# Optimization experiments

Measured on AMD Instinct MI355X. Metric: run time of the kernel, lower is better.

## Reference

```python
import jax, jax.numpy as jnp
import numpy as np

B, L, D, H = 4, 8192, 1024, 8
Dh = D // H
EPS = 1e-4
PAD = 1  # circular padding on each side, kernel_size=3, stride=1


def setup_inputs() -> dict:
    key = jax.random.key(0)
    k1, k2, k3, k4, k5 = jax.random.split(key, 5)
    return {
        "x": jax.random.normal(k1, (B, L, D), dtype=jnp.float32),
        "hash_w": jax.random.normal(k2, (H, Dh, 2), dtype=jnp.float32) * 0.05,
        "hash_b": jax.random.normal(k3, (H, 2), dtype=jnp.float32) * 0.05,
        "conv_w": jax.random.normal(k4, (D, D // H, 3), dtype=jnp.float32) * 0.05,
        "conv_b": jax.random.normal(k5, (D,), dtype=jnp.float32) * 0.05,
    }


def reference(x, hash_w, hash_b, conv_w, conv_b):
    # x: [B, L, D]
    xh = x.reshape(B, L, H, Dh)
    # per-head 2-dim hash projection, concatenated as [x0,y0,x1,y1,...] on last dim
    proj = jnp.einsum('blhd,hdk->blhk', xh, hash_w) + hash_b  # [B,L,H,2]
    proj = proj.reshape(B, L, 2 * H)
    # faithful to torch.split(projected, n_heads, dim=2): first H vs last H channels
    h_x, h_y = proj[..., :H], proj[..., H:]
    angles = jnp.arctan(h_x / (h_y + EPS))  # [B,L,H]
    idx = jnp.argsort(angles, axis=1)       # [B,L,H] permutation along L per (b,h)
    # gather: reorder tokens per head
    xs = jnp.take_along_axis(xh, idx[..., None], axis=1)  # [B,L,H,Dh]
    # grouped circular Conv1d over the sorted sequence
    xc = xs.reshape(B, L, D).swapaxes(1, 2)               # [B,D,L]
    xc = jnp.pad(xc, ((0, 0), (0, 0), (PAD, PAD)), mode='wrap')
    y = jax.lax.conv_general_dilated(
        xc, conv_w, window_strides=(1,), padding='VALID',
        dimension_numbers=('NCH', 'OIH', 'NCH'), feature_group_count=H)
    y = y + conv_b[None, :, None]                          # [B,D,L]
    y = y.swapaxes(1, 2).reshape(B, L, H, Dh)
    # scatter back to original token order == gather with inverse permutation
    inv = jnp.argsort(idx, axis=1)
    out = jnp.take_along_axis(y, inv[..., None], axis=1)
    return out.reshape(B, L, D)
```

## Files before the change

### kernel.cpp

```cpp
#include <hip/hip_runtime.h>
#include <math.h>

#define LL 8192
#define DD 1024
#define DH 128

typedef unsigned long long u64;
typedef __attribute__((ext_vector_type(8))) short bf16x8;
typedef __attribute__((ext_vector_type(4))) float f32x4;

__device__ __forceinline__ unsigned f2bf(float f) {
  unsigned u = __float_as_uint(f);
  u = (u + 0x7fffu + ((u >> 16) & 1u)) >> 16;
  return u;
}

__device__ __forceinline__ float fdlibm_atanf(float x) {
#pragma clang fp contract(off)
  const float atanhi0 = __uint_as_float(0x3eed6338u);
  const float atanhi1 = __uint_as_float(0x3f490fdau);
  const float atanhi2 = __uint_as_float(0x3f7b985eu);
  const float atanhi3 = __uint_as_float(0x3fc90fdau);
  const float atanlo0 = __uint_as_float(0x31ac3769u);
  const float atanlo1 = __uint_as_float(0x33222168u);
  const float atanlo2 = __uint_as_float(0x33140fb4u);
  const float atanlo3 = __uint_as_float(0x33a22168u);
  const float aT0 = __uint_as_float(0x3eaaaaa9u);
  const float aT1 = __uint_as_float(0xbe4cca98u);
  const float aT2 = __uint_as_float(0x3e11f50du);
  const float aT3 = __uint_as_float(0xbdda1247u);
  const float aT4 = __uint_as_float(0x3d7cac25u);
  unsigned hx = __float_as_uint(x);
  unsigned ix = hx & 0x7fffffffu;
  int id;
  if (ix >= 0x4c800000u) {
    if (ix > 0x7f800000u) return x + x;
    float z = atanhi3 + atanlo3;
    return (hx >> 31) ? -z : z;
  }
  if (ix < 0x3ee00000u) {
    if (ix < 0x39800000u) return x;
    id = -1;
  } else {
    x = fabsf(x);
    if (ix < 0x3f980000u) {
      if (ix < 0x3f300000u) { id = 0; x = (2.0f * x - 1.0f) / (2.0f + x); }
      else                  { id = 1; x = (x - 1.0f) / (x + 1.0f); }
    } else {
      if (ix < 0x401c0000u) { id = 2; x = (x - 1.5f) / (1.0f + 1.5f * x); }
      else                  { id = 3; x = -1.0f / x; }
    }
  }
  float z = x * x;
  float w = z * z;
  float s1 = z * (aT0 + w * (aT2 + w * aT4));
  float s2 = w * (aT1 + w * aT3);
  if (id < 0) return x - x * (s1 + s2);
  float r;
  if (id == 0)      r = atanhi0 - ((x * (s1 + s2) - atanlo0) - x);
  else if (id == 1) r = atanhi1 - ((x * (s1 + s2) - atanlo1) - x);
  else if (id == 2) r = atanhi2 - ((x * (s1 + s2) - atanlo2) - x);
  else              r = atanhi3 - ((x * (s1 + s2) - atanlo3) - x);
  return (hx >> 31) ? -r : r;
}

__global__ __launch_bounds__(256) void k_keys(const float* __restrict__ x,
                                              const float* __restrict__ hw,
                                              const float* __restrict__ hb,
                                              u64* __restrict__ ks,
                                              const float* __restrict__ cw,
                                              unsigned short* __restrict__ wb) {
  __shared__ float2 wL[128][8];
  __shared__ float projL[32][16];
  const int tid = threadIdx.x;
  const float2* hw2 = (const float2*)hw;
  for (int i = tid; i < 1024; i += 256) {
    int hh = i >> 7, dd = i & 127;
    wL[dd][hh] = hw2[i];
  }
  __syncthreads();
  const int r = tid >> 3;
  const int h = tid & 7;
  const int m = blockIdx.x * 32 + r;
  const int b = m >> 13, l = m & (LL - 1);
  const float4* xp = (const float4*)(x + (size_t)m * DD + h * DH);
  float a0 = 0.f, a1 = 0.f;
#pragma unroll
  for (int q = 0; q < 32; ++q) {
    float4 v = xp[q];
    float2 w0 = wL[q * 4 + 0][h];
    float2 w1 = wL[q * 4 + 1][h];
    float2 w2 = wL[q * 4 + 2][h];
    float2 w3 = wL[q * 4 + 3][h];
    a0 = fmaf(v.x, w0.x, a0); a1 = fmaf(v.x, w0.y, a1);
    a0 = fmaf(v.y, w1.x, a0); a1 = fmaf(v.y, w1.y, a1);
    a0 = fmaf(v.z, w2.x, a0); a1 = fmaf(v.z, w2.y, a1);
    a0 = fmaf(v.w, w3.x, a0); a1 = fmaf(v.w, w3.y, a1);
  }
  projL[r][h * 2 + 0] = a0;
  projL[r][h * 2 + 1] = a1;
  __syncthreads();
  const int j = h;
  float px = projL[r][j] + hb[j];
  float py = projL[r][8 + j] + hb[8 + j];
  float den = py + 1e-4f;
  float ratio = px / den;
  float angle = fdlibm_atanf(ratio);
  unsigned am = __float_as_uint(angle);
  am = (am & 0x80000000u) ? ~am : (am | 0x80000000u);
  ks[((size_t)b * 8 + j) * LL + l] = ((u64)am << 13) | (u64)l;
  {
    int base = blockIdx.x * 384;
    for (int g = base + tid; g < base + 384; g += 256) {
      int hh = g / 49152;
      int rem = g % 49152;
      int kk = rem >> 12;
      int rem2 = rem & 4095;
      int n = rem2 >> 9;
      int rem3 = rem2 & 511;
      int l2 = rem3 >> 3;
      int j2 = rem3 & 7;
      int k = kk * 32 + ((l2 >> 4) * 8) + j2;
      int o = n * 16 + (l2 & 15);
      int t = k >> 7, i2 = k & 127;
      wb[g] = (unsigned short)f2bf(cw[((size_t)(hh * 128 + o)) * 384 + i2 * 3 + t]);
    }
  }
}

__global__ __launch_bounds__(256) void k_sort_loc512(u64* __restrict__ ks) {
  __shared__ u64 sk[512];
  const int blk = blockIdx.x;
  const int seg = blk >> 4, c = blk & 15;
  u64* base = ks + (size_t)seg * LL + c * 512;
  const int tid = threadIdx.x;
  sk[tid] = base[tid];
  sk[tid + 256] = base[tid + 256];
  __syncthreads();
  const int cb = c * 512;
  for (int size = 2; size <= 512; size <<= 1) {
    for (int stride = size >> 1; stride > 0; stride >>= 1) {
      int i = 2 * tid - (tid & (stride - 1));
      int j = i + stride;
      bool up = (((cb + i) & size) == 0);
      u64 a = sk[i], d = sk[j];
      if ((a > d) == up) { sk[i] = d; sk[j] = a; }
      __syncthreads();
    }
  }
  base[tid] = sk[tid];
  base[tid + 256] = sk[tid + 256];
}

__global__ __launch_bounds__(1024) void k_sort_loc2k(u64* __restrict__ ks) {
  __shared__ u64 sk[2048];
  const int blk = blockIdx.x;
  const int seg = blk >> 2, c = blk & 3;
  u64* base = ks + (size_t)seg * LL + c * 2048;
  const int tid = threadIdx.x;
  sk[tid] = base[tid];
  sk[tid + 1024] = base[tid + 1024];
  __syncthreads();
  const int cb = c * 2048;
  for (int size = 1024; size <= 2048; size <<= 1) {
    for (int stride = size >> 1; stride > 0; stride >>= 1) {
      int i = 2 * tid - (tid & (stride - 1));
      int j = i + stride;
      bool up = (((cb + i) & size) == 0);
      u64 a = sk[i], d = sk[j];
      if ((a > d) == up) { sk[i] = d; sk[j] = a; }
      __syncthreads();
    }
  }
  base[tid] = sk[tid];
  base[tid + 1024] = sk[tid + 1024];
}

__global__ __launch_bounds__(1024) void k_sort_t4k(u64* __restrict__ ks) {
  __shared__ u64 sk[4096];
  const int blk = blockIdx.x;
  const int seg = blk >> 1, c = blk & 1;
  u64* base = ks + (size_t)seg * LL + c * 4096;
  const int tid = threadIdx.x;
#pragma unroll
  for (int i = 0; i < 4; ++i) sk[tid + i * 1024] = base[tid + i * 1024];
  __syncthreads();
  const int cb = c * 4096;
  for (int stride = 2048; stride > 0; stride >>= 1) {
#pragma unroll
    for (int pp = 0; pp < 2; ++pp) {
      int p = tid + pp * 1024;
      int i = 2 * p - (p & (stride - 1));
      int j = i + stride;
      bool up = (((cb + i) & 4096) == 0);
      u64 a = sk[i], d = sk[j];
      if ((a > d) == up) { sk[i] = d; sk[j] = a; }
    }
    __syncthreads();
  }
#pragma unroll
  for (int i = 0; i < 4; ++i) base[tid + i * 1024] = sk[tid + i * 1024];
}

__global__ __launch_bounds__(1024) void k_sort_tailg8(const u64* __restrict__ ks,
                                                      int* __restrict__ perm) {
  __shared__ u64 sk[2048];
  const int blk = blockIdx.x;
  const int seg = blk >> 2, c = blk & 3;
  const u64* base = ks + (size_t)seg * LL;
  const int tid = threadIdx.x;
#pragma unroll
  for (int s = 0; s < 2; ++s) {
    int i = tid + s * 1024;
    u64 e0 = base[i], e1 = base[i + 2048], e2 = base[i + 4096], e3 = base[i + 6144];
    u64 tt;
    if (e0 > e2) { tt = e0; e0 = e2; e2 = tt; }
    if (e1 > e3) { tt = e1; e1 = e3; e3 = tt; }
    if (e0 > e1) { tt = e0; e0 = e1; e1 = tt; }
    if (e2 > e3) { tt = e2; e2 = e3; e3 = tt; }
    sk[i] = (c == 0) ? e0 : (c == 1) ? e1 : (c == 2) ? e2 : e3;
  }
  __syncthreads();
  for (int stride = 1024; stride > 0; stride >>= 1) {
    int i = 2 * tid - (tid & (stride - 1));
    int j = i + stride;
    u64 a = sk[i], d = sk[j];
    if (a > d) { sk[i] = d; sk[j] = a; }
    __syncthreads();
  }
  int* dst = perm + (size_t)seg * LL + c * 2048;
  dst[tid] = (int)(sk[tid] & (u64)(LL - 1));
  dst[tid + 1024] = (int)(sk[tid + 1024] & (u64)(LL - 1));
}

__global__ __launch_bounds__(256) void k_conv(const float* __restrict__ x,
                                              const unsigned short* __restrict__ wb,
                                              const float* __restrict__ bias,
                                              const int* __restrict__ perm,
                                              float* __restrict__ out) {
  __shared__ short Xs[66 * 136];
  __shared__ short Ws[8 * 64 * 8];
  __shared__ int Ps2[66];
  const int tid = threadIdx.x;
  const int bid = blockIdx.x;
  const int tile = bid & 127;
  const int h = (bid >> 7) & 7;
  const int b = bid >> 10;
  const int r0 = tile * 64;
  const int* pbh = perm + ((size_t)b * 8 + h) * LL;
  if (tid < 66) Ps2[tid] = pbh[(r0 + tid - 1 + LL) & (LL - 1)];
  const uint4* wsrc = (const uint4*)(wb + (size_t)h * 49152);
  uint4 wr0 = wsrc[tid];
  uint4 wr1 = wsrc[tid + 256];
  __syncthreads();
  {
    const int ln = tid & 31;
    for (int j = (tid >> 5); j < 66; j += 8) {
      int src = Ps2[j];
      float4 v = ((const float4*)(x + ((size_t)(b * LL + src)) * DD + h * DH))[ln];
      uint2 pk;
      pk.x = f2bf(v.x) | (f2bf(v.y) << 16);
      pk.y = f2bf(v.z) | (f2bf(v.w) << 16);
      *(uint2*)(Xs + j * 136 + ln * 4) = pk;
    }
  }
  const int w = tid >> 6;
  const int l = tid & 63;
  const int arow = w * 16 + (l & 15);
  const int acol = (l >> 4) * 8;
  f32x4 acc[8];
#pragma unroll
  for (int n = 0; n < 8; ++n) acc[n] = (f32x4){0.f, 0.f, 0.f, 0.f};
  uint4* Ws16 = (uint4*)Ws;
  for (int kk = 0; kk < 12; ++kk) {
    __syncthreads();
    Ws16[tid] = wr0;
    Ws16[tid + 256] = wr1;
    __syncthreads();
    if (kk < 11) {
      wr0 = wsrc[(kk + 1) * 512 + tid];
      wr1 = wsrc[(kk + 1) * 512 + tid + 256];
    }
    bf16x8 af = *(const bf16x8*)(Xs + (arow + (kk >> 2)) * 136 + (kk & 3) * 32 + acol);
#pragma unroll
    for (int n = 0; n < 8; ++n) {
      bf16x8 bf_ = *(const bf16x8*)(Ws + (n * 64 + l) * 8);
      acc[n] = __builtin_amdgcn_mfma_f32_16x16x32_bf16(af, bf_, acc[n], 0, 0, 0);
    }
  }
  int dsts[4];
#pragma unroll
  for (int reg = 0; reg < 4; ++reg) dsts[reg] = Ps2[1 + w * 16 + (l >> 4) * 4 + reg];
#pragma unroll
  for (int n = 0; n < 8; ++n) {
    int o = h * DH + n * 16 + (l & 15);
    float bv = bias[o];
#pragma unroll
    for (int reg = 0; reg < 4; ++reg) {
      out[((size_t)(b * LL + dsts[reg])) * DD + o] = acc[n][reg] + bv;
    }
  }
}

extern "C" void kernel_launch(void* const* d_in, const int* in_sizes, int n_in,
                              void* d_out, int out_size, void* d_ws, size_t ws_size,
                              hipStream_t stream) {
  const float* x  = (const float*)d_in[0];
  const float* hw = (const float*)d_in[1];
  const float* hb = (const float*)d_in[2];
  const float* cw = (const float*)d_in[3];
  const float* cb = (const float*)d_in[4];
  float* out = (float*)d_out;
  u64* ks   = (u64*)d_ws;
  int* perm = (int*)((char*)d_ws + (2u << 20));
  unsigned short* wbp = (unsigned short*)((char*)d_ws + (3u << 20));

  k_keys<<<1024, 256, 0, stream>>>(x, hw, hb, ks, cw, wbp);
  k_sort_loc512<<<512, 256, 0, stream>>>(ks);
  k_sort_loc2k<<<128, 1024, 0, stream>>>(ks);
  k_sort_t4k<<<64, 1024, 0, stream>>>(ks);
  k_sort_tailg8<<<128, 1024, 0, stream>>>(ks, perm);
  k_conv<<<4096, 256, 0, stream>>>(x, wbp, cb, perm, out);
}
```

Baseline: 118.3 us.

## Cache bf16 per-head copy of x in keys kernel for conv gather

The keys kernel, which already reads all of x, now also converts it to bf16 and writes a head-major [B,H,L,Dh] copy into workspace, staged through a swizzled shared-memory tile for coalesced stores. The conv kernel then gathers permuted rows from this half-size contiguous copy instead of re-reading fp32 x and converting. This halves the bytes the gather reads, at the cost of an extra 64 MB write plus 64 KB of LDS in the keys kernel, which may lower its occupancy. It falls back to the old path if the workspace is too small.

```diff
diff --git a/kernel.cpp b/kernel.cpp
--- a/kernel.cpp
+++ b/kernel.cpp
@@ -64,14 +64,17 @@
   return (hx >> 31) ? -r : r;
 }
 
+template <int XC>
 __global__ __launch_bounds__(256) void k_keys(const float* __restrict__ x,
                                               const float* __restrict__ hw,
                                               const float* __restrict__ hb,
                                               u64* __restrict__ ks,
                                               const float* __restrict__ cw,
-                                              unsigned short* __restrict__ wb) {
+                                              unsigned short* __restrict__ wb,
+                                              unsigned short* __restrict__ xc) {
   __shared__ float2 wL[128][8];
   __shared__ float projL[32][16];
+  __shared__ short Xl[XC ? 32 * 1024 : 8];
   const int tid = threadIdx.x;
   const float2* hw2 = (const float2*)hw;
   for (int i = tid; i < 1024; i += 256) {
@@ -84,10 +87,24 @@
   const int m = blockIdx.x * 32 + r;
   const int b = m >> 13, l = m & (LL - 1);
   const float4* xp = (const float4*)(x + (size_t)m * DD + h * DH);
+  const int swt = ((r & 3) * 4 + (h >> 1));
   float a0 = 0.f, a1 = 0.f;
+  unsigned pvx = 0, pvy = 0;
 #pragma unroll
   for (int q = 0; q < 32; ++q) {
     float4 v = xp[q];
+    if (XC) {
+      unsigned cx = f2bf(v.x) | (f2bf(v.y) << 16);
+      unsigned cy = f2bf(v.z) | (f2bf(v.w) << 16);
+      if ((q & 1) == 0) { pvx = cx; pvy = cy; }
+      else {
+        uint4 o;
+        if (h & 1) { o.x = cx; o.y = cy; o.z = pvx; o.w = pvy; }
+        else       { o.x = pvx; o.y = pvy; o.z = cx; o.w = cy; }
+        int pe = (q >> 1) ^ swt;
+        *(uint4*)(Xl + r * 1024 + h * 128 + pe * 8) = o;
+      }
+    }
     float2 w0 = wL[q * 4 + 0][h];
     float2 w1 = wL[q * 4 + 1][h];
     float2 w2 = wL[q * 4 + 2][h];
@@ -109,6 +126,25 @@
   unsigned am = __float_as_uint(angle);
   am = (am & 0x80000000u) ? ~am : (am | 0x80000000u);
   ks[((size_t)b * 8 + j) * LL + l] = ((u64)am << 13) | (u64)l;
+  if (XC) {
+    const int m0 = blockIdx.x * 32;
+    const int b0 = m0 >> 13, l0 = m0 & (LL - 1);
+    const int a = tid & 15;
+#pragma unroll
+    for (int c = 0; c < 8; ++c) {
+      unsigned short* slab = xc + ((size_t)(b0 * 8 + c) * LL + l0) * DH;
+#pragma unroll
+      for (int pass = 0; pass < 2; ++pass) {
+        int lr = (tid >> 4) + pass * 16;
+        int tr = (lr * 4 + (c >> 1)) & 15;
+        uint4 v = *(const uint4*)(Xl + lr * 1024 + c * 128 + ((a ^ tr) * 8));
+        uint4 o;
+        if (c & 1) { o.x = v.z; o.y = v.w; o.z = v.x; o.w = v.y; }
+        else       { o = v; }
+        *(uint4*)(slab + lr * 128 + a * 8) = o;
+      }
+    }
+  }
   {
     int base = blockIdx.x * 384;
     for (int g = base + tid; g < base + 384; g += 256) {
@@ -233,7 +269,9 @@
   dst[tid + 1024] = (int)(sk[tid + 1024] & (u64)(LL - 1));
 }
 
+template <int XC>
 __global__ __launch_bounds__(256) void k_conv(const float* __restrict__ x,
+                                              const unsigned short* __restrict__ xc,
                                               const unsigned short* __restrict__ wb,
                                               const float* __restrict__ bias,
                                               const int* __restrict__ perm,
@@ -255,13 +293,21 @@
   __syncthreads();
   {
     const int ln = tid & 31;
-    for (int j = (tid >> 5); j < 66; j += 8) {
-      int src = Ps2[j];
-      float4 v = ((const float4*)(x + ((size_t)(b * LL + src)) * DD + h * DH))[ln];
-      uint2 pk;
-      pk.x = f2bf(v.x) | (f2bf(v.y) << 16);
-      pk.y = f2bf(v.z) | (f2bf(v.w) << 16);
-      *(uint2*)(Xs + j * 136 + ln * 4) = pk;
+    if (XC) {
+      const unsigned short* xcb = xc + ((size_t)(b * 8 + h)) * LL * DH;
+      for (int j = (tid >> 5); j < 66; j += 8) {
+        const uint2* sp = (const uint2*)(xcb + (size_t)Ps2[j] * DH);
+        *(uint2*)(Xs + j * 136 + ln * 4) = sp[ln];
+      }
+    } else {
+      for (int j = (tid >> 5); j < 66; j += 8) {
+        int src = Ps2[j];
+        float4 v = ((const float4*)(x + ((size_t)(b * LL + src)) * DD + h * DH))[ln];
+        uint2 pk;
+        pk.x = f2bf(v.x) | (f2bf(v.y) << 16);
+        pk.y = f2bf(v.z) | (f2bf(v.w) << 16);
+        *(uint2*)(Xs + j * 136 + ln * 4) = pk;
+      }
     }
   }
   const int w = tid >> 6;
@@ -314,11 +360,17 @@
   u64* ks   = (u64*)d_ws;
   int* perm = (int*)((char*)d_ws + (2u << 20));
   unsigned short* wbp = (unsigned short*)((char*)d_ws + (3u << 20));
-
-  k_keys<<<1024, 256, 0, stream>>>(x, hw, hb, ks, cw, wbp);
+  const size_t XC_OFF = (size_t)4 << 20;
+  const size_t XC_BYTES = (size_t)4 * 8 * LL * DH * 2;
+  bool use_xc = ws_size >= XC_OFF + XC_BYTES;
+  unsigned short* xcp = (unsigned short*)((char*)d_ws + XC_OFF);
+
+  if (use_xc) k_keys<1><<<1024, 256, 0, stream>>>(x, hw, hb, ks, cw, wbp, xcp);
+  else        k_keys<0><<<1024, 256, 0, stream>>>(x, hw, hb, ks, cw, wbp, nullptr);
   k_sort_loc512<<<512, 256, 0, stream>>>(ks);
   k_sort_loc2k<<<128, 1024, 0, stream>>>(ks);
   k_sort_t4k<<<64, 1024, 0, stream>>>(ks);
   k_sort_tailg8<<<128, 1024, 0, stream>>>(ks, perm);
-  k_conv<<<4096, 256, 0, stream>>>(x, wbp, cb, perm, out);
-}
+  if (use_xc) k_conv<1><<<4096, 256, 0, stream>>>(x, xcp, wbp, cb, perm, out);
+  else        k_conv<0><<<4096, 256, 0, stream>>>(x, nullptr, wbp, cb, perm, out);
+}
```

After: 134.1 us. 1.13x slower.
